# Kernel tuning notes

Hardware: AMD Instinct MI355X
Metric: run time of the kernel (lower is better)

The kernel has to match this reference:

```python
import jax, jax.numpy as jnp
import numpy as np

B, L, T, D, H, DH = 8, 1024, 1024, 768, 12, 64
SPATIAL_DIM = 5


def setup_inputs() -> dict:
    key = jax.random.key(0)
    ks = jax.random.split(key, 12)
    scale = 1.0 / np.sqrt(D)
    inp = {
        "q": jax.random.normal(ks[0], (B, L, D), dtype=jnp.float32),
        "k": jax.random.normal(ks[1], (B, T, D), dtype=jnp.float32),
        "v": jax.random.normal(ks[2], (B, T, D), dtype=jnp.float32),
        "pairwise_locs": jax.random.normal(ks[3], (B, L, T, SPATIAL_DIM), dtype=jnp.float32),
        # last 64 key positions are padding in every batch row (never all-True)
        "key_padding_mask": jnp.broadcast_to(jnp.arange(T) >= T - 64, (B, T)),
        "Wq": jax.random.normal(ks[4], (D, H * DH), dtype=jnp.float32) * scale,
        "bq": jnp.zeros((H * DH,), dtype=jnp.float32),
        "Wk": jax.random.normal(ks[5], (D, H * DH), dtype=jnp.float32) * scale,
        "bk": jnp.zeros((H * DH,), dtype=jnp.float32),
        "Wv": jax.random.normal(ks[6], (D, H * DH), dtype=jnp.float32) * scale,
        "bv": jnp.zeros((H * DH,), dtype=jnp.float32),
        "Wo": jax.random.normal(ks[7], (H * DH, D), dtype=jnp.float32) * scale,
        "bo": jnp.zeros((D,), dtype=jnp.float32),
    }
    return inp


def reference(q, k, v, pairwise_locs, key_padding_mask, Wq, bq, Wk, bk, Wv, bv, Wo, bo):
    # pairwise_locs is accepted but unused in this forward path (as in the source).
    b, l, _ = q.shape
    t = k.shape[1]
    qh = (q @ Wq + bq).reshape(b, l, H, DH)  # b l h d
    kh = (k @ Wk + bk).reshape(b, t, H, DH)  # b t h d
    vh = (v @ Wv + bv).reshape(b, t, H, DH)  # b t h d
    attn = jnp.einsum('blhd,bthd->bhlt', qh, kh) / jnp.sqrt(jnp.float32(DH))
    attn = jnp.where(key_padding_mask[:, None, None, :], -jnp.inf, attn)
    fused_attn = jax.nn.softmax(attn, axis=-1)
    out = jnp.einsum('bhlt,bthd->blhd', fused_attn, vh).reshape(b, l, H * DH)
    return out @ Wo + bo  # dropout is identity in eval mode
```

## Files before the change

kernel.cpp:

```cpp
#include <hip/hip_runtime.h>
#include <hip/hip_bf16.h>
#include <cstdint>
#include <cstddef>
#include <cmath>

#define NB 8
#define NL 1024
#define NT 1024
#define ND 768
#define NH 12
#define NDH 64
#define NM (NB*NL)

typedef short short8 __attribute__((ext_vector_type(8)));
typedef unsigned short ushort4v __attribute__((ext_vector_type(4)));
typedef unsigned int uint4v __attribute__((ext_vector_type(4)));
typedef unsigned int uint2v __attribute__((ext_vector_type(2)));
typedef float f32x4 __attribute__((ext_vector_type(4)));
typedef float float4v __attribute__((ext_vector_type(4)));

__device__ __forceinline__ unsigned short f2bf(float f) {
  union { __hip_bfloat16 h; unsigned short u; } cv;
  cv.h = __float2bfloat16(f);
  return cv.u;
}
__device__ __forceinline__ unsigned pk2(float lo, float hi) {
  return (unsigned)f2bf(lo) | ((unsigned)f2bf(hi) << 16);
}
__device__ __forceinline__ f32x4 vmax4(f32x4 a, f32x4 b) {
  f32x4 r;
  r[0] = fmaxf(a[0], b[0]); r[1] = fmaxf(a[1], b[1]);
  r[2] = fmaxf(a[2], b[2]); r[3] = fmaxf(a[3], b[3]);
  return r;
}
__device__ __forceinline__ void gll16(const void* g, void* l) {
  __builtin_amdgcn_global_load_lds(
      (const __attribute__((address_space(1))) unsigned int*)g,
      (__attribute__((address_space(3))) unsigned int*)l, 16, 0, 0);
}

__global__ __launch_bounds__(256) void wt_kernel(
    const float* __restrict__ W0, const float* __restrict__ W1,
    const float* __restrict__ W2, const float* __restrict__ W3,
    unsigned short* __restrict__ Wt) {
  __shared__ float tile[32][33];
  const float* W = blockIdx.z == 0 ? W0 : blockIdx.z == 1 ? W1 : blockIdx.z == 2 ? W2 : W3;
  const int k0 = blockIdx.x * 32, n0 = blockIdx.y * 32;
  const int tx = threadIdx.x & 31, ty = threadIdx.x >> 5;
  for (int r = ty; r < 32; r += 8) tile[r][tx] = W[(size_t)(k0 + r) * ND + n0 + tx];
  __syncthreads();
  unsigned short* out = Wt + (size_t)blockIdx.z * ND * ND;
  for (int r = ty; r < 32; r += 8) out[(size_t)(n0 + r) * ND + k0 + tx] = f2bf(tile[tx][r]);
}

template<int MODE>
__global__ __launch_bounds__(256) void gemm_kernel(
    const float* __restrict__ Af0, const float* __restrict__ Af1,
    const unsigned short* __restrict__ Ab, const unsigned short* __restrict__ Wt,
    const float* __restrict__ bias0, const float* __restrict__ bias1,
    unsigned short* __restrict__ outb0, unsigned short* __restrict__ outb1,
    float* __restrict__ outf) {
  __shared__ __align__(16) unsigned short As[128 * 64];
  __shared__ __align__(16) unsigned short Bs[128 * 64];
  const int tid = threadIdx.x, lane = tid & 63, w = tid >> 6;
  const int c = lane & 15, g = lane >> 4;
  const int wrow = w & 1, wcol = w >> 1;
  const int l8 = lane >> 3, l7 = lane & 7, csw = l7 ^ l8;
  const int mbase = blockIdx.x * 128, nbase = blockIdx.y * 128;
  const int z = (MODE == 0) ? blockIdx.z : MODE;

  const float* Af = (MODE == 0) ? (z == 0 ? Af0 : Af1) : Af0;
  const unsigned short* Bt = Wt + (size_t)z * ND * ND;
  const float* bias = (MODE == 0 && z == 1) ? bias1 : bias0;

  f32x4 acc[4][4];
#pragma unroll
  for (int m = 0; m < 4; m++)
#pragma unroll
    for (int n = 0; n < 4; n++) acc[m][n] = (f32x4){0.f, 0.f, 0.f, 0.f};

  for (int k0 = 0; k0 < ND; k0 += 64) {
    if (MODE != 3) {
#pragma unroll
      for (int i = 0; i < 4; i++) {
        int id = i * 256 + tid;
        int r = id >> 3, cc = id & 7;
        const float* src = &Af[(size_t)(mbase + r) * ND + k0 + cc * 8];
        float4v x0 = *(const float4v*)src;
        float4v x1 = *(const float4v*)(src + 4);
        uint4v y = {pk2(x0[0], x0[1]), pk2(x0[2], x0[3]),
                    pk2(x1[0], x1[1]), pk2(x1[2], x1[3])};
        *(uint4v*)&As[r * 64 + ((cc ^ (r & 7)) * 8)] = y;
      }
    } else {
#pragma unroll
      for (int it = 0; it < 4; it++) {
        int r = it * 32 + w * 8 + l8;
        gll16(&Ab[(size_t)(mbase + r) * ND + k0 + csw * 8], &As[(it * 32 + w * 8) * 64]);
      }
    }
#pragma unroll
    for (int it = 0; it < 4; it++) {
      int r = it * 32 + w * 8 + l8;
      gll16(&Bt[(size_t)(nbase + r) * ND + k0 + csw * 8], &Bs[(it * 32 + w * 8) * 64]);
    }
    __syncthreads();

#pragma unroll
    for (int ks = 0; ks < 2; ks++) {
      short8 a[4], b[4];
#pragma unroll
      for (int m = 0; m < 4; m++) {
        int r = wrow * 64 + m * 16 + c;
        a[m] = *(const short8*)&As[r * 64 + (((ks * 4 + g) ^ (c & 7)) * 8)];
      }
#pragma unroll
      for (int n = 0; n < 4; n++) {
        int r = wcol * 64 + n * 16 + c;
        b[n] = *(const short8*)&Bs[r * 64 + (((ks * 4 + g) ^ (c & 7)) * 8)];
      }
#pragma unroll
      for (int m = 0; m < 4; m++)
#pragma unroll
        for (int n = 0; n < 4; n++) {
          if (MODE == 2)
            acc[m][n] = __builtin_amdgcn_mfma_f32_16x16x32_bf16(a[m], b[n], acc[m][n], 0, 0, 0);
          else
            acc[m][n] = __builtin_amdgcn_mfma_f32_16x16x32_bf16(b[n], a[m], acc[m][n], 0, 0, 0);
        }
    }
    __syncthreads();
  }

  if (MODE == 2) {
#pragma unroll
    for (int n = 0; n < 4; n++) {
      const int col = nbase + wcol * 64 + n * 16 + c;
      const float bv = bias[col];
      const int h = col >> 6, dd = col & 63;
#pragma unroll
      for (int m = 0; m < 4; m++) {
        const int r0 = mbase + wrow * 64 + m * 16 + g * 4;
        const int bb = r0 >> 10, t = r0 & (NT - 1);
        ushort4v y;
#pragma unroll
        for (int j = 0; j < 4; j++) y[j] = f2bf(acc[m][n][j] + bv);
        *(ushort4v*)&outb0[((size_t)(bb * NH + h) * NDH + dd) * NT + t] = y;
      }
    }
  } else {
    const float scale = (MODE == 0 && z == 0) ? 0.125f * 1.44269504f : 1.0f;
    unsigned short* outb = (MODE == 0) ? (z == 0 ? outb0 : outb1) : nullptr;
#pragma unroll
    for (int n = 0; n < 4; n++) {
      const int colb = nbase + wcol * 64 + n * 16 + g * 4;
      float4v bv4 = *(const float4v*)&bias[colb];
#pragma unroll
      for (int m = 0; m < 4; m++) {
        const int row = mbase + wrow * 64 + m * 16 + c;
        if (MODE == 3) {
          float4v y;
#pragma unroll
          for (int j = 0; j < 4; j++) y[j] = acc[m][n][j] + bv4[j];
          *(float4v*)&outf[(size_t)row * ND + colb] = y;
        } else {
          ushort4v y;
#pragma unroll
          for (int j = 0; j < 4; j++) y[j] = f2bf((acc[m][n][j] + bv4[j]) * scale);
          *(ushort4v*)&outb[(size_t)row * ND + colb] = y;
        }
      }
    }
  }
}

__global__ __launch_bounds__(256) void attn_kernel(
    const unsigned short* __restrict__ qh, const unsigned short* __restrict__ kh,
    const unsigned short* __restrict__ vhT, const unsigned int* __restrict__ mask,
    unsigned short* __restrict__ ao) {
  __shared__ __align__(16) unsigned short Ks[2][64 * 64];
  __shared__ __align__(16) unsigned short Vs[2][64 * 64];
  __shared__ __align__(16) unsigned short Ps[4][32][72];
  const int tid = threadIdx.x, lane = tid & 63, w = tid >> 6;
  const int c = lane & 15, g = lane >> 4;
  const int l8 = lane >> 3, l7 = lane & 7, csw = l7 ^ l8;
  const int qb = blockIdx.x * 128;
  const int b = blockIdx.y / NH, h = blockIdx.y % NH;
  const size_t kbase = (size_t)b * NT * ND + h * NDH;
  const size_t vbase = (size_t)(b * NH + h) * NDH * NT;

  short8 aq[2][2];
#pragma unroll
  for (int half = 0; half < 2; half++) {
    size_t qrow = (size_t)(b * NL + qb + w * 32 + half * 16 + c) * ND + h * NDH;
#pragma unroll
    for (int ks = 0; ks < 2; ks++)
      aq[half][ks] = *(const short8*)&qh[qrow + ks * 32 + g * 8];
  }

  f32x4 o[2][4], lrv[2];
#pragma unroll
  for (int half = 0; half < 2; half++) {
    lrv[half] = (f32x4){0.f, 0.f, 0.f, 0.f};
#pragma unroll
    for (int f = 0; f < 4; f++) o[half][f] = (f32x4){0.f, 0.f, 0.f, 0.f};
  }
  float mr[2] = {-1e30f, -1e30f};

#pragma unroll
  for (int it = 0; it < 2; it++) {
    int r = w * 16 + it * 8 + l8;
    gll16(&kh[kbase + (size_t)r * ND + csw * 8], &Ks[0][(w * 16 + it * 8) * 64]);
    gll16(&vhT[vbase + (size_t)r * NT + csw * 8], &Vs[0][(w * 16 + it * 8) * 64]);
  }
  __syncthreads();

  for (int t0 = 0; t0 < NT; t0 += 64) {
    const int cur = (t0 >> 6) & 1;
    if (t0 + 64 < NT) {
#pragma unroll
      for (int it = 0; it < 2; it++) {
        int r = w * 16 + it * 8 + l8;
        gll16(&kh[kbase + (size_t)(t0 + 64 + r) * ND + csw * 8],
              &Ks[cur ^ 1][(w * 16 + it * 8) * 64]);
        gll16(&vhT[vbase + (size_t)r * NT + (t0 + 64) + csw * 8],
              &Vs[cur ^ 1][(w * 16 + it * 8) * 64]);
      }
    }

    unsigned long long tm = __ballot(mask[(size_t)b * NT + t0 + lane] != 0u);

    if (tm != ~0ull) {
      f32x4 s[2][4];
#pragma unroll
      for (int half = 0; half < 2; half++)
#pragma unroll
        for (int n = 0; n < 4; n++) s[half][n] = (f32x4){0.f, 0.f, 0.f, 0.f};
      __builtin_amdgcn_s_setprio(1);
#pragma unroll
      for (int ks = 0; ks < 2; ks++)
#pragma unroll
        for (int n = 0; n < 4; n++) {
          short8 ak = *(const short8*)&Ks[cur][(n * 16 + c) * 64 + (((ks * 4 + g) ^ (c & 7)) * 8)];
          s[0][n] = __builtin_amdgcn_mfma_f32_16x16x32_bf16(ak, aq[0][ks], s[0][n], 0, 0, 0);
          s[1][n] = __builtin_amdgcn_mfma_f32_16x16x32_bf16(ak, aq[1][ks], s[1][n], 0, 0, 0);
        }
      __builtin_amdgcn_s_setprio(0);

      if (tm) {
        unsigned long long tms = tm >> (g * 4);
#pragma unroll
        for (int n = 0; n < 4; n++)
#pragma unroll
          for (int j = 0; j < 4; j++)
            if ((tms >> (n * 16 + j)) & 1) { s[0][n][j] = -INFINITY; s[1][n][j] = -INFINITY; }
      }

      float mt[2];
#pragma unroll
      for (int half = 0; half < 2; half++) {
        f32x4 mv = vmax4(vmax4(s[half][0], s[half][1]), vmax4(s[half][2], s[half][3]));
        mt[half] = fmaxf(fmaxf(mv[0], mv[1]), fmaxf(mv[2], mv[3]));
      }
      bool ok = (mt[0] <= mr[0] + 8.f) && (mt[1] <= mr[1] + 8.f);
      if (!__all(ok)) {
#pragma unroll
        for (int half = 0; half < 2; half++) {
          float mrow = mt[half];
          mrow = fmaxf(mrow, __shfl_xor(mrow, 16, 64));
          mrow = fmaxf(mrow, __shfl_xor(mrow, 32, 64));
          float mnew = fmaxf(mr[half], mrow);
          float alpha = exp2f(mr[half] - mnew);
          mr[half] = mnew;
#pragma unroll
          for (int j = 0; j < 4; j++) lrv[half][j] *= alpha;
#pragma unroll
          for (int f = 0; f < 4; f++)
#pragma unroll
            for (int j = 0; j < 4; j++) o[half][f][j] *= alpha;
        }
      }

#pragma unroll
      for (int half = 0; half < 2; half++) {
#pragma unroll
        for (int n = 0; n < 4; n++) {
#pragma unroll
          for (int j = 0; j < 4; j++) s[half][n][j] = exp2f(s[half][n][j] - mr[half]);
          lrv[half] += s[half][n];
        }
        unsigned* pr = (unsigned*)&Ps[w][half * 16 + c][0];
#pragma unroll
        for (int n = 0; n < 4; n++) {
          uint2v y = {pk2(s[half][n][0], s[half][n][1]), pk2(s[half][n][2], s[half][n][3])};
          *(uint2v*)&pr[n * 8 + g * 2] = y;
        }
      }

      __builtin_amdgcn_s_setprio(1);
#pragma unroll
      for (int ks = 0; ks < 2; ks++) {
        short8 bp0 = *(const short8*)&Ps[w][c][ks * 32 + g * 8];
        short8 bp1 = *(const short8*)&Ps[w][16 + c][ks * 32 + g * 8];
#pragma unroll
        for (int f = 0; f < 4; f++) {
          short8 av = *(const short8*)&Vs[cur][(f * 16 + c) * 64 + (((ks * 4 + g) ^ (c & 7)) * 8)];
          o[0][f] = __builtin_amdgcn_mfma_f32_16x16x32_bf16(av, bp0, o[0][f], 0, 0, 0);
          o[1][f] = __builtin_amdgcn_mfma_f32_16x16x32_bf16(av, bp1, o[1][f], 0, 0, 0);
        }
      }
      __builtin_amdgcn_s_setprio(0);
    }
    __syncthreads();
  }

#pragma unroll
  for (int half = 0; half < 2; half++) {
    float lr = (lrv[half][0] + lrv[half][1]) + (lrv[half][2] + lrv[half][3]);
    lr += __shfl_xor(lr, 16, 64);
    lr += __shfl_xor(lr, 32, 64);
    float inv = 1.f / lr;
    size_t row = (size_t)(b * NL + qb + w * 32 + half * 16 + c) * ND + h * NDH;
#pragma unroll
    for (int f = 0; f < 4; f++) {
      ushort4v y;
#pragma unroll
      for (int j = 0; j < 4; j++) y[j] = f2bf(o[half][f][j] * inv);
      *(ushort4v*)&ao[row + f * 16 + g * 4] = y;
    }
  }
}

extern "C" void kernel_launch(void* const* d_in, const int* in_sizes, int n_in,
                              void* d_out, int out_size, void* d_ws, size_t ws_size,
                              hipStream_t stream) {
  const float* q  = (const float*)d_in[0];
  const float* k  = (const float*)d_in[1];
  const float* v  = (const float*)d_in[2];
  const unsigned int* mask = (const unsigned int*)d_in[4];
  const float* Wq = (const float*)d_in[5];
  const float* bq = (const float*)d_in[6];
  const float* Wk = (const float*)d_in[7];
  const float* bk = (const float*)d_in[8];
  const float* Wv = (const float*)d_in[9];
  const float* bv = (const float*)d_in[10];
  const float* Wo = (const float*)d_in[11];
  const float* bo = (const float*)d_in[12];
  float* out = (float*)d_out;

  unsigned short* ws  = (unsigned short*)d_ws;
  unsigned short* Wt  = ws;
  unsigned short* qhb = Wt + (size_t)4 * ND * ND;
  unsigned short* khb = qhb + (size_t)NM * ND;
  unsigned short* vhT = khb + (size_t)NM * ND;
  unsigned short* aob = vhT + (size_t)NM * ND;

  wt_kernel<<<dim3(ND / 32, ND / 32, 4), 256, 0, stream>>>(Wq, Wk, Wv, Wo, Wt);

  gemm_kernel<0><<<dim3(NM / 128, ND / 128, 2), 256, 0, stream>>>(
      q, k, nullptr, Wt, bq, bk, qhb, khb, nullptr);
  gemm_kernel<2><<<dim3(NM / 128, ND / 128), 256, 0, stream>>>(
      v, nullptr, nullptr, Wt, bv, nullptr, vhT, nullptr, nullptr);

  attn_kernel<<<dim3(NL / 128, NB * NH), 256, 0, stream>>>(qhb, khb, vhT, mask, aob);

  gemm_kernel<3><<<dim3(NM / 128, ND / 128), 256, 0, stream>>>(
      nullptr, nullptr, aob, Wt, bo, nullptr, nullptr, nullptr, out);
}
```

Baseline: 168.5 us.

## Merge QKV projection launches and split attention tiles into 32-key substeps

The Q/K projection launch and the V projection launch are merged into one grid with z=3, so all three GEMMs run concurrently in a single launch. The attention inner loop now processes each 64-key tile as two 32-key subtiles. Fully masked 32-key halves are skipped, and P goes through a smaller XOR-swizzled shared buffer instead of a padded one. In exchange there is more per-subtile softmax and max-check overhead, plus a runtime branch on z inside the GEMM MFMA loop.

New measurement: 170.2 us. Within noise of the previous version (+1.0%).

```diff
diff --git a/kernel.cpp b/kernel.cpp
--- a/kernel.cpp
+++ b/kernel.cpp
@@ -56,10 +56,12 @@
 template<int MODE>
 __global__ __launch_bounds__(256) void gemm_kernel(
     const float* __restrict__ Af0, const float* __restrict__ Af1,
-    const unsigned short* __restrict__ Ab, const unsigned short* __restrict__ Wt,
+    const float* __restrict__ Af2, const unsigned short* __restrict__ Ab,
+    const unsigned short* __restrict__ Wt,
     const float* __restrict__ bias0, const float* __restrict__ bias1,
+    const float* __restrict__ bias2,
     unsigned short* __restrict__ outb0, unsigned short* __restrict__ outb1,
-    float* __restrict__ outf) {
+    unsigned short* __restrict__ outb2, float* __restrict__ outf) {
   __shared__ __align__(16) unsigned short As[128 * 64];
   __shared__ __align__(16) unsigned short Bs[128 * 64];
   const int tid = threadIdx.x, lane = tid & 63, w = tid >> 6;
@@ -67,11 +69,11 @@
   const int wrow = w & 1, wcol = w >> 1;
   const int l8 = lane >> 3, l7 = lane & 7, csw = l7 ^ l8;
   const int mbase = blockIdx.x * 128, nbase = blockIdx.y * 128;
-  const int z = (MODE == 0) ? blockIdx.z : MODE;
-
-  const float* Af = (MODE == 0) ? (z == 0 ? Af0 : Af1) : Af0;
+  const int z = (MODE == 0) ? blockIdx.z : 3;
+
+  const float* Af = (MODE == 0) ? (z == 0 ? Af0 : z == 1 ? Af1 : Af2) : nullptr;
   const unsigned short* Bt = Wt + (size_t)z * ND * ND;
-  const float* bias = (MODE == 0 && z == 1) ? bias1 : bias0;
+  const float* bias = (MODE == 0) ? (z == 0 ? bias0 : z == 1 ? bias1 : bias2) : bias0;
 
   f32x4 acc[4][4];
 #pragma unroll
@@ -80,7 +82,7 @@
     for (int n = 0; n < 4; n++) acc[m][n] = (f32x4){0.f, 0.f, 0.f, 0.f};
 
   for (int k0 = 0; k0 < ND; k0 += 64) {
-    if (MODE != 3) {
+    if (MODE == 0) {
 #pragma unroll
       for (int i = 0; i < 4; i++) {
         int id = i * 256 + tid;
@@ -119,20 +121,24 @@
         int r = wcol * 64 + n * 16 + c;
         b[n] = *(const short8*)&Bs[r * 64 + (((ks * 4 + g) ^ (c & 7)) * 8)];
       }
-#pragma unroll
-      for (int m = 0; m < 4; m++)
-#pragma unroll
-        for (int n = 0; n < 4; n++) {
-          if (MODE == 2)
+      if (MODE == 0 && z == 2) {
+#pragma unroll
+        for (int m = 0; m < 4; m++)
+#pragma unroll
+          for (int n = 0; n < 4; n++)
             acc[m][n] = __builtin_amdgcn_mfma_f32_16x16x32_bf16(a[m], b[n], acc[m][n], 0, 0, 0);
-          else
+      } else {
+#pragma unroll
+        for (int m = 0; m < 4; m++)
+#pragma unroll
+          for (int n = 0; n < 4; n++)
             acc[m][n] = __builtin_amdgcn_mfma_f32_16x16x32_bf16(b[n], a[m], acc[m][n], 0, 0, 0);
-        }
+      }
     }
     __syncthreads();
   }
 
-  if (MODE == 2) {
+  if (MODE == 0 && z == 2) {
 #pragma unroll
     for (int n = 0; n < 4; n++) {
       const int col = nbase + wcol * 64 + n * 16 + c;
@@ -145,7 +151,7 @@
         ushort4v y;
 #pragma unroll
         for (int j = 0; j < 4; j++) y[j] = f2bf(acc[m][n][j] + bv);
-        *(ushort4v*)&outb0[((size_t)(bb * NH + h) * NDH + dd) * NT + t] = y;
+        *(ushort4v*)&outb2[((size_t)(bb * NH + h) * NDH + dd) * NT + t] = y;
       }
     }
   } else {
@@ -180,10 +186,11 @@
     unsigned short* __restrict__ ao) {
   __shared__ __align__(16) unsigned short Ks[2][64 * 64];
   __shared__ __align__(16) unsigned short Vs[2][64 * 64];
-  __shared__ __align__(16) unsigned short Ps[4][32][72];
+  __shared__ __align__(16) unsigned short Ps[4][32 * 32];
   const int tid = threadIdx.x, lane = tid & 63, w = tid >> 6;
   const int c = lane & 15, g = lane >> 4;
-  const int l8 = lane >> 3, l7 = lane & 7, csw = l7 ^ l8;
+  const int l8 = lane >> 3, l7 = lane & 7;
+  const int swz4 = (c & 3) ^ ((c >> 2) & 3);
   const int qb = blockIdx.x * 128;
   const int b = blockIdx.y / NH, h = blockIdx.y % NH;
   const size_t kbase = (size_t)b * NT * ND + h * NDH;
@@ -210,106 +217,108 @@
 #pragma unroll
   for (int it = 0; it < 2; it++) {
     int r = w * 16 + it * 8 + l8;
-    gll16(&kh[kbase + (size_t)r * ND + csw * 8], &Ks[0][(w * 16 + it * 8) * 64]);
-    gll16(&vhT[vbase + (size_t)r * NT + csw * 8], &Vs[0][(w * 16 + it * 8) * 64]);
+    int cs = l7 ^ (r & 7);
+    gll16(&kh[kbase + (size_t)r * ND + cs * 8], &Ks[0][(w * 16 + it * 8) * 64]);
+    gll16(&vhT[vbase + (size_t)r * NT + cs * 8], &Vs[0][(w * 16 + it * 8) * 64]);
   }
   __syncthreads();
 
-  for (int t0 = 0; t0 < NT; t0 += 64) {
-    const int cur = (t0 >> 6) & 1;
-    if (t0 + 64 < NT) {
+  for (int g0 = 0; g0 < NT; g0 += 64) {
+    const int cur = (g0 >> 6) & 1;
+    if (g0 + 64 < NT) {
 #pragma unroll
       for (int it = 0; it < 2; it++) {
         int r = w * 16 + it * 8 + l8;
-        gll16(&kh[kbase + (size_t)(t0 + 64 + r) * ND + csw * 8],
+        int cs = l7 ^ (r & 7);
+        gll16(&kh[kbase + (size_t)(g0 + 64 + r) * ND + cs * 8],
               &Ks[cur ^ 1][(w * 16 + it * 8) * 64]);
-        gll16(&vhT[vbase + (size_t)r * NT + (t0 + 64) + csw * 8],
+        gll16(&vhT[vbase + (size_t)r * NT + (g0 + 64) + cs * 8],
               &Vs[cur ^ 1][(w * 16 + it * 8) * 64]);
       }
     }
 
-    unsigned long long tm = __ballot(mask[(size_t)b * NT + t0 + lane] != 0u);
-
-    if (tm != ~0ull) {
-      f32x4 s[2][4];
-#pragma unroll
-      for (int half = 0; half < 2; half++)
-#pragma unroll
-        for (int n = 0; n < 4; n++) s[half][n] = (f32x4){0.f, 0.f, 0.f, 0.f};
-      __builtin_amdgcn_s_setprio(1);
-#pragma unroll
-      for (int ks = 0; ks < 2; ks++)
-#pragma unroll
-        for (int n = 0; n < 4; n++) {
-          short8 ak = *(const short8*)&Ks[cur][(n * 16 + c) * 64 + (((ks * 4 + g) ^ (c & 7)) * 8)];
-          s[0][n] = __builtin_amdgcn_mfma_f32_16x16x32_bf16(ak, aq[0][ks], s[0][n], 0, 0, 0);
-          s[1][n] = __builtin_amdgcn_mfma_f32_16x16x32_bf16(ak, aq[1][ks], s[1][n], 0, 0, 0);
-        }
-      __builtin_amdgcn_s_setprio(0);
-
-      if (tm) {
-        unsigned long long tms = tm >> (g * 4);
-#pragma unroll
-        for (int n = 0; n < 4; n++)
-#pragma unroll
-          for (int j = 0; j < 4; j++)
-            if ((tms >> (n * 16 + j)) & 1) { s[0][n][j] = -INFINITY; s[1][n][j] = -INFINITY; }
-      }
-
-      float mt[2];
-#pragma unroll
-      for (int half = 0; half < 2; half++) {
-        f32x4 mv = vmax4(vmax4(s[half][0], s[half][1]), vmax4(s[half][2], s[half][3]));
-        mt[half] = fmaxf(fmaxf(mv[0], mv[1]), fmaxf(mv[2], mv[3]));
-      }
-      bool ok = (mt[0] <= mr[0] + 8.f) && (mt[1] <= mr[1] + 8.f);
-      if (!__all(ok)) {
+    unsigned long long tm = __ballot(mask[(size_t)b * NT + g0 + lane] != 0u);
+
+#pragma unroll
+    for (int sub = 0; sub < 2; sub++) {
+      unsigned tmw = (unsigned)(tm >> (sub * 32));
+      if (tmw != 0xffffffffu) {
+        f32x4 s[2][2];
+#pragma unroll
+        for (int half = 0; half < 2; half++)
+#pragma unroll
+          for (int n = 0; n < 2; n++) s[half][n] = (f32x4){0.f, 0.f, 0.f, 0.f};
+        __builtin_amdgcn_s_setprio(1);
+#pragma unroll
+        for (int ks = 0; ks < 2; ks++)
+#pragma unroll
+          for (int n = 0; n < 2; n++) {
+            short8 ak = *(const short8*)&Ks[cur][(sub * 32 + n * 16 + c) * 64 +
+                                                (((ks * 4 + g) ^ (c & 7)) * 8)];
+            s[0][n] = __builtin_amdgcn_mfma_f32_16x16x32_bf16(ak, aq[0][ks], s[0][n], 0, 0, 0);
+            s[1][n] = __builtin_amdgcn_mfma_f32_16x16x32_bf16(ak, aq[1][ks], s[1][n], 0, 0, 0);
+          }
+        __builtin_amdgcn_s_setprio(0);
+
+        if (tmw) {
+#pragma unroll
+          for (int n = 0; n < 2; n++)
+#pragma unroll
+            for (int j = 0; j < 4; j++)
+              if ((tmw >> (n * 16 + g * 4 + j)) & 1) { s[0][n][j] = -INFINITY; s[1][n][j] = -INFINITY; }
+        }
+
+        float mt[2];
 #pragma unroll
         for (int half = 0; half < 2; half++) {
-          float mrow = mt[half];
-          mrow = fmaxf(mrow, __shfl_xor(mrow, 16, 64));
-          mrow = fmaxf(mrow, __shfl_xor(mrow, 32, 64));
-          float mnew = fmaxf(mr[half], mrow);
-          float alpha = exp2f(mr[half] - mnew);
-          mr[half] = mnew;
-#pragma unroll
-          for (int j = 0; j < 4; j++) lrv[half][j] *= alpha;
-#pragma unroll
-          for (int f = 0; f < 4; f++)
-#pragma unroll
-            for (int j = 0; j < 4; j++) o[half][f][j] *= alpha;
-        }
-      }
-
-#pragma unroll
-      for (int half = 0; half < 2; half++) {
-#pragma unroll
-        for (int n = 0; n < 4; n++) {
-#pragma unroll
-          for (int j = 0; j < 4; j++) s[half][n][j] = exp2f(s[half][n][j] - mr[half]);
-          lrv[half] += s[half][n];
-        }
-        unsigned* pr = (unsigned*)&Ps[w][half * 16 + c][0];
-#pragma unroll
-        for (int n = 0; n < 4; n++) {
-          uint2v y = {pk2(s[half][n][0], s[half][n][1]), pk2(s[half][n][2], s[half][n][3])};
-          *(uint2v*)&pr[n * 8 + g * 2] = y;
-        }
-      }
-
-      __builtin_amdgcn_s_setprio(1);
-#pragma unroll
-      for (int ks = 0; ks < 2; ks++) {
-        short8 bp0 = *(const short8*)&Ps[w][c][ks * 32 + g * 8];
-        short8 bp1 = *(const short8*)&Ps[w][16 + c][ks * 32 + g * 8];
+          f32x4 mv = vmax4(s[half][0], s[half][1]);
+          mt[half] = fmaxf(fmaxf(mv[0], mv[1]), fmaxf(mv[2], mv[3]));
+        }
+        bool ok = (mt[0] <= mr[0] + 8.f) && (mt[1] <= mr[1] + 8.f);
+        if (!__all(ok)) {
+#pragma unroll
+          for (int half = 0; half < 2; half++) {
+            float mrow = mt[half];
+            mrow = fmaxf(mrow, __shfl_xor(mrow, 16, 64));
+            mrow = fmaxf(mrow, __shfl_xor(mrow, 32, 64));
+            float mnew = fmaxf(mr[half], mrow);
+            float alpha = exp2f(mr[half] - mnew);
+            mr[half] = mnew;
+#pragma unroll
+            for (int j = 0; j < 4; j++) lrv[half][j] *= alpha;
+#pragma unroll
+            for (int f = 0; f < 4; f++)
+#pragma unroll
+              for (int j = 0; j < 4; j++) o[half][f][j] *= alpha;
+          }
+        }
+
+#pragma unroll
+        for (int half = 0; half < 2; half++) {
+#pragma unroll
+          for (int n = 0; n < 2; n++) {
+#pragma unroll
+            for (int j = 0; j < 4; j++) s[half][n][j] = exp2f(s[half][n][j] - mr[half]);
+            lrv[half] += s[half][n];
+            uint2v y = {pk2(s[half][n][0], s[half][n][1]),
+                        pk2(s[half][n][2], s[half][n][3])};
+            *(uint2v*)&Ps[w][(half * 16 + c) * 32 +
+                             (((2 * n + (g >> 1)) ^ swz4) * 8) + (g & 1) * 4] = y;
+          }
+        }
+
+        __builtin_amdgcn_s_setprio(1);
+        short8 bp0 = *(const short8*)&Ps[w][c * 32 + ((g ^ swz4) * 8)];
+        short8 bp1 = *(const short8*)&Ps[w][(16 + c) * 32 + ((g ^ swz4) * 8)];
 #pragma unroll
         for (int f = 0; f < 4; f++) {
-          short8 av = *(const short8*)&Vs[cur][(f * 16 + c) * 64 + (((ks * 4 + g) ^ (c & 7)) * 8)];
+          short8 av = *(const short8*)&Vs[cur][(f * 16 + c) * 64 +
+                                              (((sub * 4 + g) ^ (c & 7)) * 8)];
           o[0][f] = __builtin_amdgcn_mfma_f32_16x16x32_bf16(av, bp0, o[0][f], 0, 0, 0);
           o[1][f] = __builtin_amdgcn_mfma_f32_16x16x32_bf16(av, bp1, o[1][f], 0, 0, 0);
         }
-      }
-      __builtin_amdgcn_s_setprio(0);
+        __builtin_amdgcn_s_setprio(0);
+      }
     }
     __syncthreads();
   }
@@ -357,13 +366,12 @@
 
   wt_kernel<<<dim3(ND / 32, ND / 32, 4), 256, 0, stream>>>(Wq, Wk, Wv, Wo, Wt);
 
-  gemm_kernel<0><<<dim3(NM / 128, ND / 128, 2), 256, 0, stream>>>(
-      q, k, nullptr, Wt, bq, bk, qhb, khb, nullptr);
-  gemm_kernel<2><<<dim3(NM / 128, ND / 128), 256, 0, stream>>>(
-      v, nullptr, nullptr, Wt, bv, nullptr, vhT, nullptr, nullptr);
+  gemm_kernel<0><<<dim3(NM / 128, ND / 128, 3), 256, 0, stream>>>(
+      q, k, v, nullptr, Wt, bq, bk, bv, qhb, khb, vhT, nullptr);
 
   attn_kernel<<<dim3(NL / 128, NB * NH), 256, 0, stream>>>(qhb, khb, vhT, mask, aob);
 
   gemm_kernel<3><<<dim3(NM / 128, ND / 128), 256, 0, stream>>>(
-      nullptr, nullptr, aob, Wt, bo, nullptr, nullptr, nullptr, out);
-}
+      nullptr, nullptr, nullptr, aob, Wt, bo, nullptr, nullptr,
+      nullptr, nullptr, nullptr, out);
+}
```
